# Optimization experiments

Hardware: AMD Instinct MI355X
Metric: run time of the kernel (lower is better)

Reference implementation:

```python
import jax, jax.numpy as jnp
import numpy as np

B, L, E, H = 4, 2048, 1024, 16
D = E // H  # head_dim = 64

def setup_inputs() -> dict:
    key = jax.random.key(0)
    ks = jax.random.split(key, 8)
    s = 1.0 / np.sqrt(E)
    return {
        "x_q": jax.random.normal(ks[0], (B, L, E), jnp.float32),
        "x_k": jax.random.normal(ks[1], (B, L, E), jnp.float32),
        "x_v": jax.random.normal(ks[2], (B, L, E), jnp.float32),
        "Wq": jax.random.uniform(ks[3], (E, E), jnp.float32, -s, s),
        "Wk": jax.random.uniform(ks[4], (E, E), jnp.float32, -s, s),
        "Wv": jax.random.uniform(ks[5], (E, E), jnp.float32, -s, s),
        "Wo": jax.random.uniform(ks[6], (E, E), jnp.float32, -s, s),
        "bo": jax.random.uniform(ks[7], (E,), jnp.float32, -s, s),
    }

def reference(x_q, x_k, x_v, Wq, Wk, Wv, Wo, bo):
    # projections (torch Linear: y = x @ W.T)
    Q = (x_q @ Wq.T).reshape(B, L, H, D).transpose(0, 2, 1, 3)  # (B,H,Lq,D)
    K = (x_k @ Wk.T).reshape(B, L, H, D).transpose(0, 2, 1, 3)
    V = (x_v @ Wv.T).reshape(B, L, H, D).transpose(0, 2, 1, 3)
    scale = 1.0 / jnp.sqrt(jnp.asarray(D, Q.dtype))
    scores = jnp.einsum('bhqd,bhkd->bhqk', Q, K) * scale  # (B,H,Lq,Lk)
    attn = jax.nn.softmax(scores, axis=-1)
    ctx = jnp.einsum('bhqk,bhkd->bhqd', attn, V)
    ctx = ctx.transpose(0, 2, 1, 3).reshape(B, L, E)
    return ctx @ Wo.T + bo
```

## Files before the change

### kernel.cpp

```cpp
#include <hip/hip_runtime.h>
#include <hip/hip_bf16.h>
#include <stdint.h>

typedef __bf16 bf16;
typedef __attribute__((ext_vector_type(8))) __bf16 bf16x8;
typedef __attribute__((ext_vector_type(4))) __bf16 bf16x4;
typedef __attribute__((ext_vector_type(4))) float f32x4;
typedef __attribute__((ext_vector_type(16))) float f32x16;
typedef __attribute__((ext_vector_type(4))) unsigned int u32x4;

#define MFMA(a, b, c) __builtin_amdgcn_mfma_f32_16x16x32_bf16(a, b, c, 0, 0, 0)
#define MFMA32(a, b, c) __builtin_amdgcn_mfma_f32_32x32x16_bf16(a, b, c, 0, 0, 0)

__device__ __forceinline__ void gload16(const void* g, void* l) {
  __builtin_amdgcn_global_load_lds(
      (const __attribute__((address_space(1))) void*)g,
      (__attribute__((address_space(3))) void*)l, 16, 0, 0);
}

__global__ void cvt4(const float* __restrict__ s0, const float* __restrict__ s1,
                     const float* __restrict__ s2, const float* __restrict__ s3,
                     bf16* __restrict__ d0, bf16* __restrict__ d1,
                     bf16* __restrict__ d2, bf16* __restrict__ d3, long n) {
  const float* s = blockIdx.y == 0 ? s0 : blockIdx.y == 1 ? s1 : blockIdx.y == 2 ? s2 : s3;
  bf16* d       = blockIdx.y == 0 ? d0 : blockIdx.y == 1 ? d1 : blockIdx.y == 2 ? d2 : d3;
  long i0 = ((long)blockIdx.x * blockDim.x + threadIdx.x) * 8;
  long gs = (long)gridDim.x * blockDim.x * 8;
  for (long i = i0; i < n; i += gs) {
    float4 a = *(const float4*)(s + i);
    float4 b = *(const float4*)(s + i + 4);
    bf16x8 ov;
    ov[0] = (bf16)a.x; ov[1] = (bf16)a.y; ov[2] = (bf16)a.z; ov[3] = (bf16)a.w;
    ov[4] = (bf16)b.x; ov[5] = (bf16)b.y; ov[6] = (bf16)b.z; ov[7] = (bf16)b.w;
    *(bf16x8*)(d + i) = ov;
  }
}

__device__ __forceinline__ void gemm_epilogue(f32x4 (&acc)[4][4], void* Cout,
                                              const float* bias, float scale,
                                              int mode, int m0, int n0, int wm,
                                              int wn, int lr, int lg) {
  for (int i = 0; i < 4; i++)
    for (int j = 0; j < 4; j++) {
      int row = m0 + wm * 64 + i * 16 + lg * 4;
      int col = n0 + wn * 64 + j * 16 + lr;
      f32x4 v = acc[i][j];
      if (mode == 2) {
        float* O = (float*)Cout;
        float bb = bias[col];
        for (int r = 0; r < 4; r++) O[(long)(row + r) * 1024 + col] = v[r] + bb;
      } else if (mode == 0) {
        bf16* O = (bf16*)Cout;
        for (int r = 0; r < 4; r++) {
          int rr = row + r;
          long idx = ((long)((rr >> 11) * 16 + (col >> 6)) * 2048 + (rr & 2047)) * 64 + (col & 63);
          O[idx] = (bf16)(v[r] * scale);
        }
      } else {
        bf16* O = (bf16*)Cout;
        long idx = ((long)((row >> 11) * 16 + (col >> 6)) * 64 + (col & 63)) * 2048 + (row & 2047);
        bf16x4 pk;
        for (int r = 0; r < 4; r++) pk[r] = (bf16)v[r];
        *(bf16x4*)(O + idx) = pk;
      }
    }
}

__global__ __launch_bounds__(256) void gemm_qkv(const float* __restrict__ xq,
                                                const float* __restrict__ xk,
                                                const float* __restrict__ xv,
                                                const bf16* __restrict__ Wb,
                                                bf16* __restrict__ Ob,
                                                float qscale) {
  __shared__ bf16 As[3][128 * 32];
  __shared__ bf16 Bs[3][128 * 32];
  const int z = blockIdx.z;
  const float* A = z == 0 ? xq : (z == 1 ? xk : xv);
  const bf16* W = Wb + (long)z * 1024 * 1024;
  bf16* O = Ob + (long)z * 8192 * 1024;
  const float scale = (z == 0) ? qscale : 1.0f;
  const int mode = (z == 2) ? 1 : 0;

  const int tid = threadIdx.x;
  const int l = tid & 63, w = tid >> 6;
  const int lr = l & 15, lg = l >> 4;
  const int lin = blockIdx.y * 8 + blockIdx.x;
  const int nl = (lin & 7) * 64 + (lin >> 3);
  const int m0 = (nl >> 3) * 128, n0 = (nl & 7) * 128;
  const int wm = w >> 1, wn = w & 1;
  f32x4 acc[4][4];
  for (int i = 0; i < 4; i++)
    for (int j = 0; j < 4; j++)
      for (int r = 0; r < 4; r++) acc[i][j][r] = 0.f;

  float4 ar0[4], ar1[4];

  auto ALOAD = [&](int kt, float4* ar) {
#pragma unroll
    for (int i = 0; i < 4; i++) {
      int c = i * 256 + tid;
      int row = c >> 3, fq = c & 7;
      ar[i] = *(const float4*)(A + (long)(m0 + row) * 1024 + kt + fq * 4);
    }
  };
  auto AWRITE = [&](const float4* ar, int buf) {
#pragma unroll
    for (int i = 0; i < 4; i++) {
      int c = i * 256 + tid;
      int row = c >> 3, fq = c & 7;
      int g = fq >> 1;
      bf16x4 pk;
      pk[0] = (bf16)ar[i].x; pk[1] = (bf16)ar[i].y;
      pk[2] = (bf16)ar[i].z; pk[3] = (bf16)ar[i].w;
      *(bf16x4*)((char*)As[buf] + row * 64 + ((g ^ ((row >> 1) & 3)) << 4) +
                 (fq & 1) * 8) = pk;
    }
  };
  auto WSTAGE = [&](int kt, int buf) {
#pragma unroll
    for (int i = 0; i < 2; i++) {
      int c = i * 256 + tid;
      int row = c >> 2, ch = c & 3;
      int g = ch ^ ((row >> 1) & 3);
      gload16(W + (long)(n0 + row) * 1024 + kt + g * 8, (char*)Bs[buf] + c * 16);
    }
  };

  ALOAD(0, ar0); WSTAGE(0, 0);
  ALOAD(32, ar1); WSTAGE(32, 1);
  asm volatile("s_waitcnt vmcnt(6)" ::: "memory");
  __builtin_amdgcn_sched_barrier(0);
  AWRITE(ar0, 0);

#pragma unroll 2
  for (int t = 0; t < 32; t++) {
    asm volatile("s_waitcnt lgkmcnt(0)" ::: "memory");
    __builtin_amdgcn_s_barrier();
    __builtin_amdgcn_sched_barrier(0);
    if (t <= 29) {
      if ((t & 1) == 0) ALOAD((t + 2) * 32, ar0);
      else              ALOAD((t + 2) * 32, ar1);
      WSTAGE((t + 2) * 32, (t + 2) % 3);
    }
    const char* Ac = (const char*)As[t % 3];
    const char* Bc = (const char*)Bs[t % 3];
    bf16x8 af[4], bw[4];
#pragma unroll
    for (int i = 0; i < 4; i++) {
      int row = wm * 64 + i * 16 + lr;
      af[i] = *(const bf16x8*)(Ac + row * 64 + ((lg ^ ((row >> 1) & 3)) << 4));
    }
#pragma unroll
    for (int j = 0; j < 4; j++) {
      int row = wn * 64 + j * 16 + lr;
      bw[j] = *(const bf16x8*)(Bc + row * 64 + ((lg ^ ((row >> 1) & 3)) << 4));
    }
#pragma unroll
    for (int i = 0; i < 4; i++)
#pragma unroll
      for (int j = 0; j < 4; j++)
        acc[i][j] = MFMA(af[i], bw[j], acc[i][j]);
    if (t <= 29)      asm volatile("s_waitcnt vmcnt(6)" ::: "memory");
    else if (t == 30) asm volatile("s_waitcnt vmcnt(0)" ::: "memory");
    __builtin_amdgcn_sched_barrier(0);
    if (t <= 30) {
      if ((t & 1) == 0) AWRITE(ar1, (t + 1) % 3);
      else              AWRITE(ar0, (t + 1) % 3);
    }
  }

  gemm_epilogue(acc, O, nullptr, scale, mode, m0, n0, wm, wn, lr, lg);
}

__global__ __launch_bounds__(256) void gemm_out(const bf16* __restrict__ A,
                                                const bf16* __restrict__ W,
                                                float* __restrict__ Cout,
                                                const float* __restrict__ bias) {
  __shared__ bf16 As[4][128 * 32];
  __shared__ bf16 Bs[4][128 * 32];
  const int tid = threadIdx.x;
  const int l = tid & 63, w = tid >> 6;
  const int lr = l & 15, lg = l >> 4;
  const int lin = blockIdx.y * 8 + blockIdx.x;
  const int nl = (lin & 7) * 64 + (lin >> 3);
  const int m0 = (nl >> 3) * 128, n0 = (nl & 7) * 128;
  const int wm = w >> 1, wn = w & 1;
  f32x4 acc[4][4];
  for (int i = 0; i < 4; i++)
    for (int j = 0; j < 4; j++)
      for (int r = 0; r < 4; r++) acc[i][j][r] = 0.f;

  auto STAGE = [&](int kt, int buf) {
#pragma unroll
    for (int i = 0; i < 2; i++) {
      int c = i * 256 + tid;
      int row = c >> 2, ch = c & 3;
      int sc = (ch ^ ((row >> 1) & 3)) * 8;
      gload16(A + (long)(m0 + row) * 1024 + kt + sc, (char*)As[0] + buf * 8192 + c * 16);
      gload16(W + (long)(n0 + row) * 1024 + kt + sc, (char*)Bs[0] + buf * 8192 + c * 16);
    }
  };

  STAGE(0, 0); STAGE(32, 1); STAGE(64, 2);

  for (int t = 0; t < 32; t++) {
    if (t <= 29)      asm volatile("s_waitcnt vmcnt(8) lgkmcnt(0)" ::: "memory");
    else if (t == 30) asm volatile("s_waitcnt vmcnt(4) lgkmcnt(0)" ::: "memory");
    else              asm volatile("s_waitcnt vmcnt(0) lgkmcnt(0)" ::: "memory");
    __builtin_amdgcn_s_barrier();
    __builtin_amdgcn_sched_barrier(0);
    const char* Ac = (const char*)As[0] + (t & 3) * 8192;
    const char* Bc = (const char*)Bs[0] + (t & 3) * 8192;
    bf16x8 af[4], bw[4];
#pragma unroll
    for (int i = 0; i < 4; i++) {
      int row = wm * 64 + i * 16 + lr;
      af[i] = *(const bf16x8*)(Ac + row * 64 + ((lg ^ ((row >> 1) & 3)) << 4));
    }
#pragma unroll
    for (int j = 0; j < 4; j++) {
      int row = wn * 64 + j * 16 + lr;
      bw[j] = *(const bf16x8*)(Bc + row * 64 + ((lg ^ ((row >> 1) & 3)) << 4));
    }
#pragma unroll
    for (int i = 0; i < 4; i++)
#pragma unroll
      for (int j = 0; j < 4; j++)
        acc[i][j] = MFMA(af[i], bw[j], acc[i][j]);
    if (t <= 28) STAGE((t + 3) * 32, (t + 3) & 3);
  }

  gemm_epilogue(acc, Cout, bias, 1.0f, 2, m0, n0, wm, wn, lr, lg);
}

__global__ __launch_bounds__(512, 4) void attn_fwd(const bf16* __restrict__ Q,
                                                   const bf16* __restrict__ K,
                                                   const bf16* __restrict__ Vt,
                                                   bf16* __restrict__ ctx) {
  __shared__ bf16 Ks[2][128 * 64];
  __shared__ bf16 Vs[2][64 * 128];
  const int tid = threadIdx.x;
  const int l = tid & 63, w = tid >> 6;
  const int q32 = l & 31, hl = l >> 5;
  const int lin = blockIdx.y * 8 + blockIdx.x;
  const int nl = (lin & 7) * 64 + (lin >> 3);
  const int bh = nl >> 3, qt = nl & 7;
  const bf16* Qh = Q + (long)bh * 2048 * 64;
  const bf16* Kh = K + (long)bh * 2048 * 64;
  const bf16* Vh = Vt + (long)bh * 64 * 2048;
  const int qb = qt * 256 + w * 32;

#define STAGE(kv0, buf)                                                          \
  {                                                                              \
    _Pragma("unroll") for (int i = 0; i < 2; i++) {                              \
      int c = i * 512 + tid;                                                     \
      int kr = c >> 3, kc = c & 7;                                               \
      gload16(Kh + (long)((kv0) + kr) * 64 + ((kc ^ (kr & 7)) << 3),             \
              (char*)Ks[buf] + c * 16);                                          \
    }                                                                            \
    _Pragma("unroll") for (int i = 0; i < 2; i++) {                              \
      int c = i * 512 + tid;                                                     \
      int r = c >> 4, v0 = c & 15;                                               \
      int vc = (v0 & 8) | ((v0 & 7) ^ (r & 7));                                  \
      gload16(Vh + (long)r * 2048 + (kv0) + vc * 8,                              \
              (char*)Vs[buf] + c * 16);                                          \
    }                                                                            \
  }

  bf16x8 bq[4];
#pragma unroll
  for (int kk = 0; kk < 4; kk++)
    bq[kk] = *(const bf16x8*)(Qh + (long)(qb + q32) * 64 + kk * 16 + hl * 8);

  f32x16 o0, o1;
#pragma unroll
  for (int r = 0; r < 16; r++) { o0[r] = 0.f; o1[r] = 0.f; }
  float lrun = 0.f;

  STAGE(0, 0);
  __syncthreads();

  for (int t = 0; t < 16; t++) {
    const int cur = t & 1;
    if (t < 15) STAGE((t + 1) * 128, cur ^ 1);
    const bf16* Kc = Ks[cur];
    const bf16* Vc = Vs[cur];
    f32x4 psum = {0.f, 0.f, 0.f, 0.f};

#pragma unroll
    for (int nn = 0; nn < 4; nn++) {
      const int row = nn * 32 + q32;
      f32x16 acc;
#pragma unroll
      for (int r = 0; r < 16; r++) acc[r] = 0.f;
      __builtin_amdgcn_s_setprio(1);
#pragma unroll
      for (int kk = 0; kk < 4; kk++) {
        int ch = (kk * 2 + hl) ^ (row & 7);
        bf16x8 ak = *(const bf16x8*)((const char*)Kc + row * 128 + (ch << 4));
        acc = MFMA32(ak, bq[kk], acc);
      }
      __builtin_amdgcn_s_setprio(0);

      f32x16 p;
#pragma unroll
      for (int r = 0; r < 16; r++) p[r] = __builtin_amdgcn_exp2f(acc[r]);
      f32x4 t4;
#pragma unroll
      for (int j = 0; j < 4; j++) t4[j] = (p[j] + p[4 + j]) + (p[8 + j] + p[12 + j]);
      psum += t4;

      unsigned wd[8];
#pragma unroll
      for (int i = 0; i < 8; i++) {
        float lo = p[2 * i], hi = p[2 * i + 1];
        asm("v_cvt_pk_bf16_f32 %0, %1, %2" : "=v"(wd[i]) : "v"(lo), "v"(hi));
      }
#pragma unroll
      for (int ss = 0; ss < 2; ss++) {
        unsigned a0 = wd[ss * 4 + 0], b0 = wd[ss * 4 + 2];
        unsigned a1 = wd[ss * 4 + 1], b1 = wd[ss * 4 + 3];
        asm("v_permlane32_swap_b32 %0, %1" : "+v"(a0), "+v"(b0));
        asm("v_permlane32_swap_b32 %0, %1" : "+v"(a1), "+v"(b1));
        u32x4 pw = {a0, a1, b0, b1};
        bf16x8 bp = *(bf16x8*)&pw;
        int ch0 = (nn * 2 + ss) * 2 + hl;
        __builtin_amdgcn_s_setprio(1);
#pragma unroll
        for (int nd = 0; nd < 2; nd++) {
          int vrw = nd * 32 + q32;
          int ch = (ch0 & 8) | ((ch0 & 7) ^ (vrw & 7));
          bf16x8 av = *(const bf16x8*)((const char*)Vc + vrw * 256 + (ch << 4));
          if (nd == 0) o0 = MFMA32(av, bp, o0);
          else         o1 = MFMA32(av, bp, o1);
        }
        __builtin_amdgcn_s_setprio(0);
      }
    }
    lrun += (psum[0] + psum[1]) + (psum[2] + psum[3]);
    __syncthreads();
  }

  lrun += __shfl_xor(lrun, 32);
  const int b = bh >> 4, h = bh & 15;
  const float inv = 1.0f / lrun;
  const int q = qb + q32;
#pragma unroll
  for (int nd = 0; nd < 2; nd++)
#pragma unroll
    for (int qd = 0; qd < 4; qd++) {
      bf16x4 pk;
#pragma unroll
      for (int r = 0; r < 4; r++)
        pk[r] = (bf16)((nd == 0 ? o0[qd * 4 + r] : o1[qd * 4 + r]) * inv);
      int d = nd * 32 + qd * 8 + hl * 4;
      *(bf16x4*)(ctx + ((long)b * 2048 + q) * 1024 + h * 64 + d) = pk;
    }
#undef STAGE
}

extern "C" void kernel_launch(void* const* d_in, const int* in_sizes, int n_in,
                              void* d_out, int out_size, void* d_ws, size_t ws_size,
                              hipStream_t stream) {
  const float* xq = (const float*)d_in[0];
  const float* xk = (const float*)d_in[1];
  const float* xv = (const float*)d_in[2];
  const float* Wq = (const float*)d_in[3];
  const float* Wk = (const float*)d_in[4];
  const float* Wv = (const float*)d_in[5];
  const float* Wo = (const float*)d_in[6];
  const float* bo = (const float*)d_in[7];

  char* p = (char*)d_ws;
  const size_t SZ_X = (size_t)8192 * 1024 * 2;
  const size_t SZ_W = (size_t)1024 * 1024 * 2;
  bf16* wqb = (bf16*)p; p += SZ_W;
  bf16* wkb = (bf16*)p; p += SZ_W;
  bf16* wvb = (bf16*)p; p += SZ_W;
  bf16* wob = (bf16*)p; p += SZ_W;
  bf16* Qb  = (bf16*)p; p += SZ_X;
  bf16* Kb  = (bf16*)p; p += SZ_X;
  bf16* Vtb = (bf16*)p; p += SZ_X;
  bf16* ctxb = (bf16*)p; p += SZ_X;
  (void)ws_size; (void)in_sizes; (void)n_in; (void)out_size;

  const float QSCALE = 0.18033688011112042f;

  cvt4<<<dim3(128, 4), 256, 0, stream>>>(Wq, Wk, Wv, Wo, wqb, wkb, wvb, wob,
                                         (long)1024 * 1024);
  gemm_qkv<<<dim3(8, 64, 3), 256, 0, stream>>>(xq, xk, xv, wqb, Qb, QSCALE);
  attn_fwd<<<dim3(8, 64), 512, 0, stream>>>(Qb, Kb, Vtb, ctxb);
  gemm_out<<<dim3(8, 64), 256, 0, stream>>>(ctxb, wob, (float*)d_out, bo);
}
```

Baseline: 189.4 us.

## Process two query tiles per wave in attention to reuse K/V LDS reads

The attention kernel now uses 256 threads per block, with each wave handling 64 query rows (two 32-row tiles) instead of 32. Each K and V fragment loaded from LDS feeds two MFMAs, which halves LDS read traffic per unit of compute. Staging loops are widened so the smaller block still fills the K/V tiles. The cost is roughly double the accumulator and register pressure and fewer waves per block, which may lower occupancy and latency hiding.

```diff
diff --git a/kernel.cpp b/kernel.cpp
--- a/kernel.cpp
+++ b/kernel.cpp
@@ -233,7 +233,7 @@
   gemm_epilogue(acc, Cout, bias, 1.0f, 2, m0, n0, wm, wn, lr, lg);
 }
 
-__global__ __launch_bounds__(512, 4) void attn_fwd(const bf16* __restrict__ Q,
+__global__ __launch_bounds__(256, 2) void attn_fwd(const bf16* __restrict__ Q,
                                                    const bf16* __restrict__ K,
                                                    const bf16* __restrict__ Vt,
                                                    bf16* __restrict__ ctx) {
@@ -248,18 +248,18 @@
   const bf16* Qh = Q + (long)bh * 2048 * 64;
   const bf16* Kh = K + (long)bh * 2048 * 64;
   const bf16* Vh = Vt + (long)bh * 64 * 2048;
-  const int qb = qt * 256 + w * 32;
+  const int qb = qt * 256 + w * 64;
 
 #define STAGE(kv0, buf)                                                          \
   {                                                                              \
-    _Pragma("unroll") for (int i = 0; i < 2; i++) {                              \
-      int c = i * 512 + tid;                                                     \
+    _Pragma("unroll") for (int i = 0; i < 4; i++) {                              \
+      int c = i * 256 + tid;                                                     \
       int kr = c >> 3, kc = c & 7;                                               \
       gload16(Kh + (long)((kv0) + kr) * 64 + ((kc ^ (kr & 7)) << 3),             \
               (char*)Ks[buf] + c * 16);                                          \
     }                                                                            \
-    _Pragma("unroll") for (int i = 0; i < 2; i++) {                              \
-      int c = i * 512 + tid;                                                     \
+    _Pragma("unroll") for (int i = 0; i < 4; i++) {                              \
+      int c = i * 256 + tid;                                                     \
       int r = c >> 4, v0 = c & 15;                                               \
       int vc = (v0 & 8) | ((v0 & 7) ^ (r & 7));                                  \
       gload16(Vh + (long)r * 2048 + (kv0) + vc * 8,                              \
@@ -267,15 +267,17 @@
     }                                                                            \
   }
 
-  bf16x8 bq[4];
-#pragma unroll
-  for (int kk = 0; kk < 4; kk++)
-    bq[kk] = *(const bf16x8*)(Qh + (long)(qb + q32) * 64 + kk * 16 + hl * 8);
-
-  f32x16 o0, o1;
-#pragma unroll
-  for (int r = 0; r < 16; r++) { o0[r] = 0.f; o1[r] = 0.f; }
-  float lrun = 0.f;
+  bf16x8 bqA[4], bqB[4];
+#pragma unroll
+  for (int kk = 0; kk < 4; kk++) {
+    bqA[kk] = *(const bf16x8*)(Qh + (long)(qb + q32) * 64 + kk * 16 + hl * 8);
+    bqB[kk] = *(const bf16x8*)(Qh + (long)(qb + 32 + q32) * 64 + kk * 16 + hl * 8);
+  }
+
+  f32x16 oA0, oA1, oB0, oB1;
+#pragma unroll
+  for (int r = 0; r < 16; r++) { oA0[r] = 0.f; oA1[r] = 0.f; oB0[r] = 0.f; oB1[r] = 0.f; }
+  float lrunA = 0.f, lrunB = 0.f;
 
   STAGE(0, 0);
   __syncthreads();
@@ -285,45 +287,55 @@
     if (t < 15) STAGE((t + 1) * 128, cur ^ 1);
     const bf16* Kc = Ks[cur];
     const bf16* Vc = Vs[cur];
-    f32x4 psum = {0.f, 0.f, 0.f, 0.f};
+    f32x4 psumA = {0.f, 0.f, 0.f, 0.f}, psumB = {0.f, 0.f, 0.f, 0.f};
 
 #pragma unroll
     for (int nn = 0; nn < 4; nn++) {
       const int row = nn * 32 + q32;
-      f32x16 acc;
-#pragma unroll
-      for (int r = 0; r < 16; r++) acc[r] = 0.f;
+      f32x16 sA, sB;
+#pragma unroll
+      for (int r = 0; r < 16; r++) { sA[r] = 0.f; sB[r] = 0.f; }
       __builtin_amdgcn_s_setprio(1);
 #pragma unroll
       for (int kk = 0; kk < 4; kk++) {
         int ch = (kk * 2 + hl) ^ (row & 7);
         bf16x8 ak = *(const bf16x8*)((const char*)Kc + row * 128 + (ch << 4));
-        acc = MFMA32(ak, bq[kk], acc);
+        sA = MFMA32(ak, bqA[kk], sA);
+        sB = MFMA32(ak, bqB[kk], sB);
       }
       __builtin_amdgcn_s_setprio(0);
 
-      f32x16 p;
-#pragma unroll
-      for (int r = 0; r < 16; r++) p[r] = __builtin_amdgcn_exp2f(acc[r]);
-      f32x4 t4;
-#pragma unroll
-      for (int j = 0; j < 4; j++) t4[j] = (p[j] + p[4 + j]) + (p[8 + j] + p[12 + j]);
-      psum += t4;
-
-      unsigned wd[8];
+#pragma unroll
+      for (int r = 0; r < 16; r++) {
+        sA[r] = __builtin_amdgcn_exp2f(sA[r]);
+        sB[r] = __builtin_amdgcn_exp2f(sB[r]);
+      }
+#pragma unroll
+      for (int j = 0; j < 4; j++) {
+        psumA[j] += (sA[j] + sA[4 + j]) + (sA[8 + j] + sA[12 + j]);
+        psumB[j] += (sB[j] + sB[4 + j]) + (sB[8 + j] + sB[12 + j]);
+      }
+
+      unsigned wdA[8], wdB[8];
 #pragma unroll
       for (int i = 0; i < 8; i++) {
-        float lo = p[2 * i], hi = p[2 * i + 1];
-        asm("v_cvt_pk_bf16_f32 %0, %1, %2" : "=v"(wd[i]) : "v"(lo), "v"(hi));
+        asm("v_cvt_pk_bf16_f32 %0, %1, %2" : "=v"(wdA[i]) : "v"(sA[2 * i]), "v"(sA[2 * i + 1]));
+        asm("v_cvt_pk_bf16_f32 %0, %1, %2" : "=v"(wdB[i]) : "v"(sB[2 * i]), "v"(sB[2 * i + 1]));
       }
 #pragma unroll
       for (int ss = 0; ss < 2; ss++) {
-        unsigned a0 = wd[ss * 4 + 0], b0 = wd[ss * 4 + 2];
-        unsigned a1 = wd[ss * 4 + 1], b1 = wd[ss * 4 + 3];
+        unsigned a0 = wdA[ss * 4 + 0], b0 = wdA[ss * 4 + 2];
+        unsigned a1 = wdA[ss * 4 + 1], b1 = wdA[ss * 4 + 3];
         asm("v_permlane32_swap_b32 %0, %1" : "+v"(a0), "+v"(b0));
         asm("v_permlane32_swap_b32 %0, %1" : "+v"(a1), "+v"(b1));
-        u32x4 pw = {a0, a1, b0, b1};
-        bf16x8 bp = *(bf16x8*)&pw;
+        u32x4 pwA = {a0, a1, b0, b1};
+        bf16x8 bpA = *(bf16x8*)&pwA;
+        unsigned c0 = wdB[ss * 4 + 0], d0 = wdB[ss * 4 + 2];
+        unsigned c1 = wdB[ss * 4 + 1], d1 = wdB[ss * 4 + 3];
+        asm("v_permlane32_swap_b32 %0, %1" : "+v"(c0), "+v"(d0));
+        asm("v_permlane32_swap_b32 %0, %1" : "+v"(c1), "+v"(d1));
+        u32x4 pwB = {c0, c1, d0, d1};
+        bf16x8 bpB = *(bf16x8*)&pwB;
         int ch0 = (nn * 2 + ss) * 2 + hl;
         __builtin_amdgcn_s_setprio(1);
 #pragma unroll
@@ -331,30 +343,35 @@
           int vrw = nd * 32 + q32;
           int ch = (ch0 & 8) | ((ch0 & 7) ^ (vrw & 7));
           bf16x8 av = *(const bf16x8*)((const char*)Vc + vrw * 256 + (ch << 4));
-          if (nd == 0) o0 = MFMA32(av, bp, o0);
-          else         o1 = MFMA32(av, bp, o1);
+          if (nd == 0) { oA0 = MFMA32(av, bpA, oA0); oB0 = MFMA32(av, bpB, oB0); }
+          else         { oA1 = MFMA32(av, bpA, oA1); oB1 = MFMA32(av, bpB, oB1); }
         }
         __builtin_amdgcn_s_setprio(0);
       }
     }
-    lrun += (psum[0] + psum[1]) + (psum[2] + psum[3]);
+    lrunA += (psumA[0] + psumA[1]) + (psumA[2] + psumA[3]);
+    lrunB += (psumB[0] + psumB[1]) + (psumB[2] + psumB[3]);
     __syncthreads();
   }
 
-  lrun += __shfl_xor(lrun, 32);
+  lrunA += __shfl_xor(lrunA, 32);
+  lrunB += __shfl_xor(lrunB, 32);
   const int b = bh >> 4, h = bh & 15;
-  const float inv = 1.0f / lrun;
-  const int q = qb + q32;
+  const float invA = 1.0f / lrunA, invB = 1.0f / lrunB;
+  const int qA = qb + q32, qB = qb + 32 + q32;
 #pragma unroll
   for (int nd = 0; nd < 2; nd++)
 #pragma unroll
     for (int qd = 0; qd < 4; qd++) {
-      bf16x4 pk;
-#pragma unroll
-      for (int r = 0; r < 4; r++)
-        pk[r] = (bf16)((nd == 0 ? o0[qd * 4 + r] : o1[qd * 4 + r]) * inv);
       int d = nd * 32 + qd * 8 + hl * 4;
-      *(bf16x4*)(ctx + ((long)b * 2048 + q) * 1024 + h * 64 + d) = pk;
+      bf16x4 pkA, pkB;
+#pragma unroll
+      for (int r = 0; r < 4; r++) {
+        pkA[r] = (bf16)((nd == 0 ? oA0[qd * 4 + r] : oA1[qd * 4 + r]) * invA);
+        pkB[r] = (bf16)((nd == 0 ? oB0[qd * 4 + r] : oB1[qd * 4 + r]) * invB);
+      }
+      *(bf16x4*)(ctx + ((long)b * 2048 + qA) * 1024 + h * 64 + d) = pkA;
+      *(bf16x4*)(ctx + ((long)b * 2048 + qB) * 1024 + h * 64 + d) = pkB;
     }
 #undef STAGE
 }
@@ -389,6 +406,6 @@
   cvt4<<<dim3(128, 4), 256, 0, stream>>>(Wq, Wk, Wv, Wo, wqb, wkb, wvb, wob,
                                          (long)1024 * 1024);
   gemm_qkv<<<dim3(8, 64, 3), 256, 0, stream>>>(xq, xk, xv, wqb, Qb, QSCALE);
-  attn_fwd<<<dim3(8, 64), 512, 0, stream>>>(Qb, Kb, Vtb, ctxb);
+  attn_fwd<<<dim3(8, 64), 256, 0, stream>>>(Qb, Kb, Vtb, ctxb);
   gemm_out<<<dim3(8, 64), 256, 0, stream>>>(ctxb, wob, (float*)d_out, bo);
 }
```

Result: no change. 190.0 us (+0.3%).
